# Performance work log

Measured on AMD Instinct MI355X. Metric: run time of the kernel, lower is better.

Reference implementation:

```python
import jax, jax.numpy as jnp
import numpy as np

B, C, N = 4, 128, 25000
E = 200000            # edges per graph
H, DH = 4, 32         # heads, per-head dim
OUT = H * DH          # 128
ED = 32               # edge feature dim


def setup_inputs() -> dict:
    key = jax.random.key(0)
    ks = jax.random.split(key, 16)
    s = 0.05
    return {
        'x': jax.random.normal(ks[0], (B, C, N, 1), jnp.float32),
        'edge_index': jax.random.randint(ks[1], (B, 2, E), 0, B * N, jnp.int64),
        'edge_attr': jax.random.normal(ks[2], (B * E, ED), jnp.float32),
        'Wq': jax.random.normal(ks[3], (C, OUT), jnp.float32) * s,
        'bq': jnp.zeros((OUT,), jnp.float32),
        'Wk': jax.random.normal(ks[4], (C, OUT), jnp.float32) * s,
        'bk': jnp.zeros((OUT,), jnp.float32),
        'Wv': jax.random.normal(ks[5], (C, OUT), jnp.float32) * s,
        'bv': jnp.zeros((OUT,), jnp.float32),
        'We': jax.random.normal(ks[6], (ED, OUT), jnp.float32) * s,
        'Wskip': jax.random.normal(ks[7], (C, OUT), jnp.float32) * s,
        'bskip': jnp.zeros((OUT,), jnp.float32),
        'W1': jax.random.normal(ks[8], (OUT, 2 * OUT), jnp.float32) * s,
        'b1': jnp.zeros((2 * OUT,), jnp.float32),
        'W2': jax.random.normal(ks[9], (2 * OUT, OUT), jnp.float32) * s,
        'b2': jnp.zeros((OUT,), jnp.float32),
    }


def reference(x, edge_index, edge_attr, Wq, bq, Wk, bk, Wv, bv, We,
              Wskip, bskip, W1, b1, W2, b2):
    b, c, n, _ = x.shape
    nb = b * n
    # [B,C,N,1] -> [B*N, C]
    xf = x.squeeze(-1).transpose(0, 2, 1).reshape(nb, c)
    # [B,2,E] -> [2, B*E]
    ei = edge_index.transpose(1, 0, 2).reshape(2, -1)
    src, dst = ei[0], ei[1]

    q = (xf @ Wq + bq).reshape(nb, H, DH)
    k = (xf @ Wk + bk).reshape(nb, H, DH)
    v = (xf @ Wv + bv).reshape(nb, H, DH)
    e = (edge_attr @ We).reshape(-1, H, DH)  # [T,H,DH]

    qi = q[dst]            # gather target queries  [T,H,DH]
    kj = k[src] + e        # gather source keys + edge proj
    vj = v[src] + e

    scale = 1.0 / np.sqrt(DH).astype(np.float32)
    alpha = (qi * kj).sum(-1) * scale  # [T,H]

    # segment softmax over edges sharing a destination node
    amax = jax.ops.segment_max(alpha, dst, num_segments=nb)
    amax = jnp.where(jnp.isfinite(amax), amax, 0.0)
    ea = jnp.exp(alpha - amax[dst])
    denom = jax.ops.segment_sum(ea, dst, num_segments=nb)
    attn = ea / (denom[dst] + 1e-16)   # [T,H]

    agg = jax.ops.segment_sum(vj * attn[..., None], dst, num_segments=nb)
    out = agg.reshape(nb, OUT) + (xf @ Wskip + bskip)  # root skip

    # feed-forward + final activation
    h = jnp.maximum(out @ W1 + b1, 0.0) @ W2 + b2
    h = jnp.maximum(h, 0.0)

    # [B*N, OUT] -> [B, OUT, N, 1]
    return h.reshape(b, n, OUT).transpose(0, 2, 1)[..., None]
```

## Files before the change

kernel.cpp:

```cpp
#include <hip/hip_runtime.h>
#include <hip/hip_bf16.h>

#define NB      100000
#define NPB     25000
#define T_E     800000
#define EPG     200000
#define DMODEL  128
#define EDIM    32
#define FFD     256
#define SCAN_NBLK 98

typedef __attribute__((ext_vector_type(8))) short bf16x8;
typedef __attribute__((ext_vector_type(4))) float f32x4;
typedef __attribute__((ext_vector_type(2))) float f32x2;

__device__ inline unsigned short f2bf(float f) {
    unsigned u = __float_as_uint(f);
    unsigned r = u + 0x7fffu + ((u >> 16) & 1u);
    return (unsigned short)(r >> 16);
}
__device__ inline unsigned pack_bf16x2(float lo, float hi) {
    return (unsigned)f2bf(lo) | ((unsigned)f2bf(hi) << 16);
}
__device__ inline float bf_lo(unsigned p) { return __uint_as_float(p << 16); }
__device__ inline float bf_hi(unsigned p) { return __uint_as_float(p & 0xffff0000u); }

__global__ __launch_bounds__(256) void k_prep(
    const float* __restrict__ W1, const float* __restrict__ W2,
    const float* __restrict__ We,
    const float* __restrict__ Wq, const float* __restrict__ Wk,
    const float* __restrict__ Wv, const float* __restrict__ Wskip,
    uint4* __restrict__ w1f, uint4* __restrict__ w2f,
    uint4* __restrict__ wef, uint4* __restrict__ wpf)
{
    int t = blockIdx.x * 256 + threadIdx.x;
    int lane = t & 63;
    int frag = t >> 6;
    if (frag >= 264) return;
    int rl = lane & 15, g = lane >> 4;
    unsigned v[4];
    if (frag < 64) {
        int m1 = frag >> 2, ks = frag & 3;
        int col1 = m1 * 16 + rl;
        int k0 = ks * 32 + g * 8;
#pragma unroll
        for (int j2 = 0; j2 < 4; ++j2) {
            float f0 = W1[(k0 + 2 * j2) * FFD + col1];
            float f1 = W1[(k0 + 2 * j2 + 1) * FFD + col1];
            v[j2] = pack_bf16x2(f0, f1);
        }
        w1f[frag * 64 + lane] = make_uint4(v[0], v[1], v[2], v[3]);
    } else if (frag < 128) {
        int f2 = frag - 64;
        int m2 = f2 >> 3, ks = f2 & 7;
        int c2 = m2 * 16 + rl;
        int k0 = ks * 32 + g * 8;
#pragma unroll
        for (int j2 = 0; j2 < 4; ++j2) {
            float f0 = W2[(k0 + 2 * j2) * DMODEL + c2];
            float f1 = W2[(k0 + 2 * j2 + 1) * DMODEL + c2];
            v[j2] = pack_bf16x2(f0, f1);
        }
        w2f[f2 * 64 + lane] = make_uint4(v[0], v[1], v[2], v[3]);
    } else if (frag < 136) {
        int m = frag - 128;
        int ocol = m * 16 + rl;
        int k0 = g * 8;
#pragma unroll
        for (int j2 = 0; j2 < 4; ++j2) {
            float f0 = We[(k0 + 2 * j2) * DMODEL + ocol];
            float f1 = We[(k0 + 2 * j2 + 1) * DMODEL + ocol];
            v[j2] = pack_bf16x2(f0, f1);
        }
        wef[m * 64 + lane] = make_uint4(v[0], v[1], v[2], v[3]);
    } else {
        int fi = frag - 136;
        int m  = fi >> 5;
        int r  = fi & 31;
        int ct = r >> 2, ks = r & 3;
        const float* W = (m == 0) ? Wq : (m == 1) ? Wk : (m == 2) ? Wv : Wskip;
        int col = ct * 16 + rl;
        int k0  = ks * 32 + g * 8;
#pragma unroll
        for (int j2 = 0; j2 < 4; ++j2) {
            float f0 = W[(k0 + 2 * j2) * DMODEL + col];
            float f1 = W[(k0 + 2 * j2 + 1) * DMODEL + col];
            v[j2] = pack_bf16x2(f0, f1);
        }
        wpf[fi * 64 + lane] = make_uint4(v[0], v[1], v[2], v[3]);
    }
}

__global__ __launch_bounds__(256) void k_proj2(
    const float* __restrict__ x, const uint4* __restrict__ wpf,
    const float* __restrict__ bq, const float* __restrict__ bk,
    const float* __restrict__ bv, const float* __restrict__ bskip,
    unsigned short* __restrict__ qb16, unsigned short* __restrict__ kvb,
    unsigned short* __restrict__ skipb16)
{
    __shared__ __align__(16) char lds[16384];
    const int tid   = threadIdx.x;
    const int node0 = blockIdx.x * 64;

    {
        const int nl   = tid & 63;
        const int half = tid >> 6;
        const int node = node0 + nl;
        const bool valid = node < NB;
        int b  = node / NPB;
        int nn = node - b * NPB;
        const float* xbase = x + (size_t)b * DMODEL * NPB + nn;
#pragma unroll
        for (int o = 0; o < 4; ++o) {
            int c0 = (half * 4 + o) * 8;
            unsigned vals[4];
#pragma unroll
            for (int j2 = 0; j2 < 4; ++j2) {
                float f0 = valid ? xbase[(size_t)(c0 + 2 * j2) * NPB] : 0.f;
                float f1 = valid ? xbase[(size_t)(c0 + 2 * j2 + 1) * NPB] : 0.f;
                vals[j2] = pack_bf16x2(f0, f1);
            }
            int byte = nl * 256 + ((c0 * 2) ^ ((nl & 7) << 4));
            *(uint4*)(&lds[byte]) = make_uint4(vals[0], vals[1], vals[2], vals[3]);
        }
    }
    __syncthreads();

    const int w = tid >> 6, lane = tid & 63;
    const int rl = lane & 15, g = lane >> 4;

    const uint4* wf = wpf + (size_t)w * 32 * 64;
    const float* bi = (w == 0) ? bq : (w == 1) ? bk : (w == 2) ? bv : bskip;
    unsigned short* base = (w == 0) ? qb16 : (w == 3) ? skipb16
                          : kvb + ((w == 2) ? 128 : 0);
    const int rowstride = (w == 1 || w == 2) ? 256 : 128;

#pragma unroll
    for (int ct = 0; ct < 8; ++ct) {
        bf16x8 A[4];
#pragma unroll
        for (int ks = 0; ks < 4; ++ks)
            A[ks] = *(const bf16x8*)&wf[(ct * 4 + ks) * 64 + lane];
        const int colb = ct * 16 + g * 4;
        const float bb0 = bi[colb], bb1 = bi[colb + 1],
                    bb2 = bi[colb + 2], bb3 = bi[colb + 3];
#pragma unroll
        for (int nt = 0; nt < 4; ++nt) {
            const int nl = nt * 16 + rl;
            f32x4 acc = {0.f, 0.f, 0.f, 0.f};
#pragma unroll
            for (int ks = 0; ks < 4; ++ks) {
                bf16x8 B = *(const bf16x8*)(&lds[nl * 256 +
                              ((ks * 64 + g * 16) ^ ((nl & 7) << 4))]);
                acc = __builtin_amdgcn_mfma_f32_16x16x32_bf16(A[ks], B, acc, 0, 0, 0);
            }
            const int node = node0 + nl;
            if (node < NB) {
                unsigned lo = pack_bf16x2(acc[0] + bb0, acc[1] + bb1);
                unsigned hi = pack_bf16x2(acc[2] + bb2, acc[3] + bb3);
                *(uint2*)&base[(size_t)node * rowstride + colb] = make_uint2(lo, hi);
            }
        }
    }
}

__global__ __launch_bounds__(256) void k_hist(
    const int* __restrict__ eidx, int* __restrict__ counts)
{
    int t = blockIdx.x * 256 + threadIdx.x;
    if (t < T_E) {
        int b = t / EPG, e = t - b * EPG;
        int dst = eidx[(size_t)(b * 2 + 1) * EPG + e];
        atomicAdd(&counts[dst], 1);
    }
}

__global__ __launch_bounds__(1024) void k_scan1(
    const int* __restrict__ counts, int* __restrict__ row_start,
    int* __restrict__ bsum)
{
    __shared__ int s[1024];
    const int tid = threadIdx.x;
    const int gid = blockIdx.x * 1024 + tid;
    int v = (gid < NB) ? counts[gid] : 0;
    s[tid] = v;
    __syncthreads();
#pragma unroll
    for (int off = 1; off < 1024; off <<= 1) {
        int tv = (tid >= off) ? s[tid - off] : 0;
        __syncthreads();
        s[tid] += tv;
        __syncthreads();
    }
    int incl = s[tid];
    if (gid < NB) row_start[gid] = incl - v;
    if (tid == 1023) bsum[blockIdx.x] = incl;
}

__global__ __launch_bounds__(128) void k_scan2(int* __restrict__ bsum)
{
    __shared__ int s[128];
    const int tid = threadIdx.x;
    int v = (tid < SCAN_NBLK) ? bsum[tid] : 0;
    s[tid] = v;
    __syncthreads();
#pragma unroll
    for (int off = 1; off < 128; off <<= 1) {
        int tv = (tid >= off) ? s[tid - off] : 0;
        __syncthreads();
        s[tid] += tv;
        __syncthreads();
    }
    if (tid < SCAN_NBLK) bsum[tid] = s[tid] - v;
}

__global__ __launch_bounds__(1024) void k_scan3(
    int* __restrict__ row_start, const int* __restrict__ bsum,
    int* __restrict__ cursor)
{
    const int gid = blockIdx.x * 1024 + threadIdx.x;
    if (gid < NB) {
        int v = row_start[gid] + bsum[blockIdx.x];
        row_start[gid] = v;
        cursor[gid] = v;
    }
}

__global__ __launch_bounds__(256) void k_scatter(
    const int* __restrict__ eidx, int* __restrict__ cursor,
    int2* __restrict__ elist2)
{
    int t = blockIdx.x * 256 + threadIdx.x;
    if (t < T_E) {
        int b = t / EPG, e = t - b * EPG;
        int dst = eidx[(size_t)(b * 2 + 1) * EPG + e];
        int src = eidx[(size_t)(b * 2) * EPG + e];
        int pos = atomicAdd(&cursor[dst], 1);
        elist2[pos] = make_int2(src, t);
    }
}

__global__ __launch_bounds__(256) void k_eproj(
    const float* __restrict__ eattr, const uint4* __restrict__ wef,
    unsigned char* __restrict__ eb)
{
    const int tid = threadIdx.x;
    const int w = tid >> 6, lane = tid & 63;
    const int rl = lane & 15, g = lane >> 4;

    bf16x8 a[8];
#pragma unroll
    for (int m = 0; m < 8; ++m) a[m] = *(const bf16x8*)&wef[m * 64 + lane];

    const int nwaves = gridDim.x * 4;
    for (int tile = blockIdx.x * 4 + w; tile < T_E / 16; tile += nwaves) {
        const float* ep = &eattr[((size_t)tile * 16 + rl) * EDIM + g * 8];
        float4 f0 = *(const float4*)ep;
        float4 f1 = *(const float4*)(ep + 4);
        uint4 bu = make_uint4(pack_bf16x2(f0.x, f0.y), pack_bf16x2(f0.z, f0.w),
                              pack_bf16x2(f1.x, f1.y), pack_bf16x2(f1.z, f1.w));
        bf16x8 b = *(bf16x8*)&bu;
        f32x4 z = {0.f, 0.f, 0.f, 0.f};
        f32x4 acc[8];
#pragma unroll
        for (int m = 0; m < 8; ++m)
            acc[m] = __builtin_amdgcn_mfma_f32_16x16x32_bf16(a[m], b, z, 0, 0, 0);
        unsigned char* out = &eb[((size_t)tile * 16 + rl) * DMODEL + g * 4];
#pragma unroll
        for (int m = 0; m < 8; ++m) {
            unsigned d = __builtin_amdgcn_cvt_pk_fp8_f32(acc[m][0], acc[m][1], 0, false);
            d = __builtin_amdgcn_cvt_pk_fp8_f32(acc[m][2], acc[m][3], d, true);
            *(unsigned*)(out + m * 16) = d;
        }
    }
}

__global__ __launch_bounds__(256) void k_aggr3(
    unsigned short* qx,
    const unsigned short* __restrict__ kvb,
    const unsigned short* __restrict__ skipb16,
    const unsigned char* __restrict__ eb,
    const int2* __restrict__ elist2,
    const int* __restrict__ row_start, const int* __restrict__ row_end)
{
    const int tid = threadIdx.x;
    const int w = tid >> 6, l = tid & 63;
    const int q4 = l >> 4;
    const int li = l & 15;
    const int c0 = li * 8;

    const int nwaves = gridDim.x * 4;
    for (int node = blockIdx.x * 4 + w; node < NB; node += nwaves) {
        const int rs = row_start[node];
        const int re = row_end[node];
        uint4 qp = *(const uint4*)&qx[(size_t)node * DMODEL + c0];
        const float q0 = bf_lo(qp.x), q1 = bf_hi(qp.x);
        const float q2 = bf_lo(qp.y), q3 = bf_hi(qp.y);
        const float q4_ = bf_lo(qp.z), q5 = bf_hi(qp.z);
        const float q6 = bf_lo(qp.w), q7 = bf_hi(qp.w);
        float a0 = 0.f, a1 = 0.f, a2 = 0.f, a3 = 0.f;
        float a4 = 0.f, a5 = 0.f, a6 = 0.f, a7 = 0.f, den = 0.f;

        for (int j0 = rs; j0 < re; j0 += 4) {
            const int jc = j0 + q4;
            const bool act = jc < re;
            uint4 kp = make_uint4(0, 0, 0, 0), vp = make_uint4(0, 0, 0, 0);
            uint2 ep8 = make_uint2(0, 0);
            if (act) {
                int2 se = elist2[jc];
                kp = *(const uint4*)&kvb[(size_t)se.x * 256 + c0];
                vp = *(const uint4*)&kvb[(size_t)se.x * 256 + 128 + c0];
                ep8 = *(const uint2*)&eb[(size_t)se.y * DMODEL + c0];
            }
            f32x2 exl = __builtin_amdgcn_cvt_pk_f32_fp8(ep8.x, false);
            f32x2 exh = __builtin_amdgcn_cvt_pk_f32_fp8(ep8.x, true);
            f32x2 eyl = __builtin_amdgcn_cvt_pk_f32_fp8(ep8.y, false);
            f32x2 eyh = __builtin_amdgcn_cvt_pk_f32_fp8(ep8.y, true);
            const float e0 = exl[0], e1 = exl[1], e2 = exh[0], e3 = exh[1];
            const float e4 = eyl[0], e5 = eyl[1], e6 = eyh[0], e7 = eyh[1];
            const float k0 = bf_lo(kp.x) + e0, k1 = bf_hi(kp.x) + e1;
            const float k2 = bf_lo(kp.y) + e2, k3 = bf_hi(kp.y) + e3;
            const float k4 = bf_lo(kp.z) + e4, k5 = bf_hi(kp.z) + e5;
            const float k6 = bf_lo(kp.w) + e6, k7 = bf_hi(kp.w) + e7;
            float p = q0 * k0 + q1 * k1 + q2 * k2 + q3 * k3
                    + q4_ * k4 + q5 * k5 + q6 * k6 + q7 * k7;
            p += __shfl_xor(p, 1, 64);
            p += __shfl_xor(p, 2, 64);
            float ea = act ? __expf(p * 0.17677669529663689f) : 0.f;
            a0 += ea * (bf_lo(vp.x) + e0);
            a1 += ea * (bf_hi(vp.x) + e1);
            a2 += ea * (bf_lo(vp.y) + e2);
            a3 += ea * (bf_hi(vp.y) + e3);
            a4 += ea * (bf_lo(vp.z) + e4);
            a5 += ea * (bf_hi(vp.z) + e5);
            a6 += ea * (bf_lo(vp.w) + e6);
            a7 += ea * (bf_hi(vp.w) + e7);
            den += ea;
        }
#pragma unroll
        for (int off = 16; off <= 32; off <<= 1) {
            a0 += __shfl_xor(a0, off, 64);
            a1 += __shfl_xor(a1, off, 64);
            a2 += __shfl_xor(a2, off, 64);
            a3 += __shfl_xor(a3, off, 64);
            a4 += __shfl_xor(a4, off, 64);
            a5 += __shfl_xor(a5, off, 64);
            a6 += __shfl_xor(a6, off, 64);
            a7 += __shfl_xor(a7, off, 64);
            den += __shfl_xor(den, off, 64);
        }
        float r = 1.0f / (den + 1e-16f);
        if (q4 == 0) {
            uint4 sp = *(const uint4*)&skipb16[(size_t)node * DMODEL + c0];
            uint4 o;
            o.x = pack_bf16x2(a0 * r + bf_lo(sp.x), a1 * r + bf_hi(sp.x));
            o.y = pack_bf16x2(a2 * r + bf_lo(sp.y), a3 * r + bf_hi(sp.y));
            o.z = pack_bf16x2(a4 * r + bf_lo(sp.z), a5 * r + bf_hi(sp.z));
            o.w = pack_bf16x2(a6 * r + bf_lo(sp.w), a7 * r + bf_hi(sp.w));
            *(uint4*)&qx[(size_t)node * DMODEL + c0] = o;
        }
    }
}

#define H1_OFF 16384

__global__ __launch_bounds__(256) void k_ffn_mfma(
    const unsigned short* __restrict__ xs16,
    const uint4* __restrict__ w1f, const float* __restrict__ b1,
    const uint4* __restrict__ w2f, const float* __restrict__ b2,
    float* __restrict__ out)
{
    __shared__ __align__(16) char lds[49152];
    const int tid   = threadIdx.x;
    const int node0 = blockIdx.x * 64;

#pragma unroll
    for (int i = 0; i < 4; ++i) {
        int linear = i * 256 + tid;
        int row = linear >> 4;
        int c8  = (linear & 15) * 8;
        int node = node0 + row;
        uint4 vv = (node < NB) ? *(const uint4*)&xs16[(size_t)node * DMODEL + c8]
                               : make_uint4(0, 0, 0, 0);
        int byte = row * 256 + ((c8 * 2) ^ ((row & 7) << 4));
        *(uint4*)(&lds[byte]) = vv;
    }
    __syncthreads();

    const int w = tid >> 6, lane = tid & 63;
    const int rl = lane & 15, g = lane >> 4;

    {
        f32x4 acc[4][4] = {};
#pragma unroll
        for (int ks = 0; ks < 4; ++ks) {
            bf16x8 a[4], b[4];
#pragma unroll
            for (int mt = 0; mt < 4; ++mt) {
                int m1 = w * 4 + mt;
                a[mt] = *(const bf16x8*)&w1f[(m1 * 4 + ks) * 64 + lane];
            }
#pragma unroll
            for (int nt = 0; nt < 4; ++nt) {
                int node = nt * 16 + rl;
                int byte = node * 256 + ((ks * 64 + g * 16) ^ ((node & 7) << 4));
                b[nt] = *(const bf16x8*)&lds[byte];
            }
#pragma unroll
            for (int mt = 0; mt < 4; ++mt)
#pragma unroll
                for (int nt = 0; nt < 4; ++nt)
                    acc[mt][nt] = __builtin_amdgcn_mfma_f32_16x16x32_bf16(
                        a[mt], b[nt], acc[mt][nt], 0, 0, 0);
        }
#pragma unroll
        for (int mt = 0; mt < 4; ++mt) {
            int col1_0 = w * 64 + mt * 16 + g * 4;
            float bb0 = b1[col1_0], bb1 = b1[col1_0 + 1],
                  bb2 = b1[col1_0 + 2], bb3 = b1[col1_0 + 3];
#pragma unroll
            for (int nt = 0; nt < 4; ++nt) {
                int node = nt * 16 + rl;
                float v0 = fmaxf(acc[mt][nt][0] + bb0, 0.f);
                float v1 = fmaxf(acc[mt][nt][1] + bb1, 0.f);
                float v2 = fmaxf(acc[mt][nt][2] + bb2, 0.f);
                float v3 = fmaxf(acc[mt][nt][3] + bb3, 0.f);
                unsigned lo = pack_bf16x2(v0, v1), hi = pack_bf16x2(v2, v3);
                int byte = H1_OFF + node * 512 + ((col1_0 * 2) ^ ((node & 7) << 4));
                *(uint2*)(&lds[byte]) = make_uint2(lo, hi);
            }
        }
    }
    __syncthreads();

    {
        f32x4 acc[2][4] = {};
#pragma unroll
        for (int ks = 0; ks < 8; ++ks) {
            bf16x8 a[2], b[4];
#pragma unroll
            for (int mt = 0; mt < 2; ++mt) {
                int m2 = w * 2 + mt;
                a[mt] = *(const bf16x8*)&w2f[(m2 * 8 + ks) * 64 + lane];
            }
#pragma unroll
            for (int nt = 0; nt < 4; ++nt) {
                int node = nt * 16 + rl;
                int byte = H1_OFF + node * 512 + ((ks * 64 + g * 16) ^ ((node & 7) << 4));
                b[nt] = *(const bf16x8*)&lds[byte];
            }
#pragma unroll
            for (int mt = 0; mt < 2; ++mt)
#pragma unroll
                for (int nt = 0; nt < 4; ++nt)
                    acc[mt][nt] = __builtin_amdgcn_mfma_f32_16x16x32_bf16(
                        a[mt], b[nt], acc[mt][nt], 0, 0, 0);
        }
#pragma unroll
        for (int mt = 0; mt < 2; ++mt) {
            int c2_0 = w * 32 + mt * 16 + g * 4;
#pragma unroll
            for (int nt = 0; nt < 4; ++nt) {
                int node = node0 + nt * 16 + rl;
                if (node < NB) {
                    int bb = node / NPB;
                    int nn = node - bb * NPB;
                    size_t base = (size_t)(bb * DMODEL) * NPB + nn;
#pragma unroll
                    for (int r = 0; r < 4; ++r) {
                        float v = fmaxf(acc[mt][nt][r] + b2[c2_0 + r], 0.f);
                        out[base + (size_t)(c2_0 + r) * NPB] = v;
                    }
                }
            }
        }
    }
}

extern "C" void kernel_launch(void* const* d_in, const int* in_sizes, int n_in,
                              void* d_out, int out_size, void* d_ws, size_t ws_size,
                              hipStream_t stream)
{
    const float* x     = (const float*)d_in[0];
    const int*   eidx  = (const int*)  d_in[1];
    const float* eattr = (const float*)d_in[2];
    const float* Wq    = (const float*)d_in[3];
    const float* bq    = (const float*)d_in[4];
    const float* Wk    = (const float*)d_in[5];
    const float* bk    = (const float*)d_in[6];
    const float* Wv    = (const float*)d_in[7];
    const float* bv    = (const float*)d_in[8];
    const float* We    = (const float*)d_in[9];
    const float* Wskip = (const float*)d_in[10];
    const float* bskip = (const float*)d_in[11];
    const float* W1    = (const float*)d_in[12];
    const float* b1    = (const float*)d_in[13];
    const float* W2    = (const float*)d_in[14];
    const float* b2    = (const float*)d_in[15];
    float* out = (float*)d_out;

    const size_t NBD = (size_t)NB * DMODEL;
    unsigned short* qb16    = (unsigned short*)d_ws;
    unsigned short* kvb     = qb16 + NBD;
    unsigned short* skipb16 = kvb + 2 * NBD;
    unsigned char*  eb      = (unsigned char*)(skipb16 + NBD);
    uint4* w1f = (uint4*)(eb + (size_t)T_E * DMODEL);
    uint4* w2f = w1f + 64 * 64;
    uint4* wef = w2f + 64 * 64;
    uint4* wpf = wef + 8 * 64;
    int* counts    = (int*)(wpf + 128 * 64);
    int* row_start = counts + NB;
    int* cursor    = row_start + NB;
    int2* elist2   = (int2*)(cursor + NB);
    int* bsum      = (int*)(elist2 + T_E);

    hipMemsetAsync(counts, 0, NB * sizeof(int), stream);
    k_prep<<<66, 256, 0, stream>>>(W1, W2, We, Wq, Wk, Wv, Wskip,
                                   w1f, w2f, wef, wpf);
    k_proj2<<<(NB + 63) / 64, 256, 0, stream>>>(x, wpf, bq, bk, bv, bskip,
                                                qb16, kvb, skipb16);
    k_hist<<<(T_E + 255) / 256, 256, 0, stream>>>(eidx, counts);
    k_scan1<<<SCAN_NBLK, 1024, 0, stream>>>(counts, row_start, bsum);
    k_scan2<<<1, 128, 0, stream>>>(bsum);
    k_scan3<<<SCAN_NBLK, 1024, 0, stream>>>(row_start, bsum, cursor);
    k_scatter<<<(T_E + 255) / 256, 256, 0, stream>>>(eidx, cursor, elist2);
    k_eproj<<<2048, 256, 0, stream>>>(eattr, wef, eb);
    k_aggr3<<<2048, 256, 0, stream>>>(qb16, kvb, skipb16, eb, elist2,
                                      row_start, cursor);
    k_ffn_mfma<<<(NB + 63) / 64, 256, 0, stream>>>(qb16, w1f, b1, w2f, b2, out);
}
```

Measured before the change: 369.1 us.

## Stage projection outputs in LDS, fuse edge scatter into eproj, unroll aggregation

```diff
diff --git a/kernel.cpp b/kernel.cpp
--- a/kernel.cpp
+++ b/kernel.cpp
@@ -91,6 +91,8 @@
     }
 }
 
+#define STG 16384
+
 __global__ __launch_bounds__(256) void k_proj2(
     const float* __restrict__ x, const uint4* __restrict__ wpf,
     const float* __restrict__ bq, const float* __restrict__ bk,
@@ -98,7 +100,7 @@
     unsigned short* __restrict__ qb16, unsigned short* __restrict__ kvb,
     unsigned short* __restrict__ skipb16)
 {
-    __shared__ __align__(16) char lds[16384];
+    __shared__ __align__(16) char lds[32768];
     const int tid   = threadIdx.x;
     const int node0 = blockIdx.x * 64;
 
@@ -129,38 +131,51 @@
     const int w = tid >> 6, lane = tid & 63;
     const int rl = lane & 15, g = lane >> 4;
 
-    const uint4* wf = wpf + (size_t)w * 32 * 64;
-    const float* bi = (w == 0) ? bq : (w == 1) ? bk : (w == 2) ? bv : bskip;
-    unsigned short* base = (w == 0) ? qb16 : (w == 3) ? skipb16
-                          : kvb + ((w == 2) ? 128 : 0);
-    const int rowstride = (w == 1 || w == 2) ? 256 : 128;
-
-#pragma unroll
-    for (int ct = 0; ct < 8; ++ct) {
-        bf16x8 A[4];
-#pragma unroll
-        for (int ks = 0; ks < 4; ++ks)
-            A[ks] = *(const bf16x8*)&wf[(ct * 4 + ks) * 64 + lane];
-        const int colb = ct * 16 + g * 4;
-        const float bb0 = bi[colb], bb1 = bi[colb + 1],
-                    bb2 = bi[colb + 2], bb3 = bi[colb + 3];
-#pragma unroll
-        for (int nt = 0; nt < 4; ++nt) {
-            const int nl = nt * 16 + rl;
-            f32x4 acc = {0.f, 0.f, 0.f, 0.f};
-#pragma unroll
-            for (int ks = 0; ks < 4; ++ks) {
-                bf16x8 B = *(const bf16x8*)(&lds[nl * 256 +
-                              ((ks * 64 + g * 16) ^ ((nl & 7) << 4))]);
-                acc = __builtin_amdgcn_mfma_f32_16x16x32_bf16(A[ks], B, acc, 0, 0, 0);
-            }
-            const int node = node0 + nl;
-            if (node < NB) {
+    for (int m = 0; m < 4; ++m) {
+        const float* bi = (m == 0) ? bq : (m == 1) ? bk : (m == 2) ? bv : bskip;
+#pragma unroll
+        for (int ct2 = 0; ct2 < 2; ++ct2) {
+            const int ct = w * 2 + ct2;
+            bf16x8 A[4];
+#pragma unroll
+            for (int ks = 0; ks < 4; ++ks)
+                A[ks] = *(const bf16x8*)&wpf[((m * 8 + ct) * 4 + ks) * 64 + lane];
+            const int colb = ct * 16 + g * 4;
+            const float bb0 = bi[colb], bb1 = bi[colb + 1],
+                        bb2 = bi[colb + 2], bb3 = bi[colb + 3];
+#pragma unroll
+            for (int nt = 0; nt < 4; ++nt) {
+                const int nl = nt * 16 + rl;
+                f32x4 acc = {0.f, 0.f, 0.f, 0.f};
+#pragma unroll
+                for (int ks = 0; ks < 4; ++ks) {
+                    bf16x8 B = *(const bf16x8*)(&lds[nl * 256 +
+                                  ((ks * 64 + g * 16) ^ ((nl & 7) << 4))]);
+                    acc = __builtin_amdgcn_mfma_f32_16x16x32_bf16(A[ks], B, acc, 0, 0, 0);
+                }
                 unsigned lo = pack_bf16x2(acc[0] + bb0, acc[1] + bb1);
                 unsigned hi = pack_bf16x2(acc[2] + bb2, acc[3] + bb3);
-                *(uint2*)&base[(size_t)node * rowstride + colb] = make_uint2(lo, hi);
-            }
-        }
+                int byte = STG + nl * 256 + ((colb * 2) ^ ((nl & 7) << 4));
+                *(uint2*)(&lds[byte]) = make_uint2(lo, hi);
+            }
+        }
+        __syncthreads();
+#pragma unroll
+        for (int i = 0; i < 4; ++i) {
+            int linear = i * 256 + tid;
+            int row = linear >> 4;
+            int c8  = (linear & 15) * 8;
+            int node = node0 + row;
+            if (node < NB) {
+                uint4 vv = *(const uint4*)(&lds[STG + row * 256 +
+                                ((c8 * 2) ^ ((row & 7) << 4))]);
+                if (m == 0)      *(uint4*)&qb16[(size_t)node * DMODEL + c8] = vv;
+                else if (m == 1) *(uint4*)&kvb[(size_t)node * 256 + c8] = vv;
+                else if (m == 2) *(uint4*)&kvb[(size_t)node * 256 + 128 + c8] = vv;
+                else             *(uint4*)&skipb16[(size_t)node * DMODEL + c8] = vv;
+            }
+        }
+        __syncthreads();
     }
 }
 
@@ -226,23 +241,10 @@
     }
 }
 
-__global__ __launch_bounds__(256) void k_scatter(
+__global__ __launch_bounds__(256) void k_escat(
+    const float* __restrict__ eattr, const uint4* __restrict__ wef,
     const int* __restrict__ eidx, int* __restrict__ cursor,
-    int2* __restrict__ elist2)
-{
-    int t = blockIdx.x * 256 + threadIdx.x;
-    if (t < T_E) {
-        int b = t / EPG, e = t - b * EPG;
-        int dst = eidx[(size_t)(b * 2 + 1) * EPG + e];
-        int src = eidx[(size_t)(b * 2) * EPG + e];
-        int pos = atomicAdd(&cursor[dst], 1);
-        elist2[pos] = make_int2(src, t);
-    }
-}
-
-__global__ __launch_bounds__(256) void k_eproj(
-    const float* __restrict__ eattr, const uint4* __restrict__ wef,
-    unsigned char* __restrict__ eb)
+    unsigned char* __restrict__ eb, int2* __restrict__ elist2)
 {
     const int tid = threadIdx.x;
     const int w = tid >> 6, lane = tid & 63;
@@ -271,6 +273,14 @@
             unsigned d = __builtin_amdgcn_cvt_pk_fp8_f32(acc[m][0], acc[m][1], 0, false);
             d = __builtin_amdgcn_cvt_pk_fp8_f32(acc[m][2], acc[m][3], d, true);
             *(unsigned*)(out + m * 16) = d;
+        }
+        if (g == 0) {
+            int t = tile * 16 + rl;
+            int bb = t / EPG, e = t - bb * EPG;
+            int dst = eidx[(size_t)(bb * 2 + 1) * EPG + e];
+            int src = eidx[(size_t)(bb * 2) * EPG + e];
+            int pos = atomicAdd(&cursor[dst], 1);
+            elist2[pos] = make_int2(src, t);
         }
     }
 }
@@ -301,52 +311,73 @@
         float a0 = 0.f, a1 = 0.f, a2 = 0.f, a3 = 0.f;
         float a4 = 0.f, a5 = 0.f, a6 = 0.f, a7 = 0.f, den = 0.f;
 
-        for (int j0 = rs; j0 < re; j0 += 4) {
-            const int jc = j0 + q4;
-            const bool act = jc < re;
-            uint4 kp = make_uint4(0, 0, 0, 0), vp = make_uint4(0, 0, 0, 0);
-            uint2 ep8 = make_uint2(0, 0);
-            if (act) {
-                int2 se = elist2[jc];
-                kp = *(const uint4*)&kvb[(size_t)se.x * 256 + c0];
-                vp = *(const uint4*)&kvb[(size_t)se.x * 256 + 128 + c0];
-                ep8 = *(const uint2*)&eb[(size_t)se.y * DMODEL + c0];
-            }
-            f32x2 exl = __builtin_amdgcn_cvt_pk_f32_fp8(ep8.x, false);
-            f32x2 exh = __builtin_amdgcn_cvt_pk_f32_fp8(ep8.x, true);
-            f32x2 eyl = __builtin_amdgcn_cvt_pk_f32_fp8(ep8.y, false);
-            f32x2 eyh = __builtin_amdgcn_cvt_pk_f32_fp8(ep8.y, true);
-            const float e0 = exl[0], e1 = exl[1], e2 = exh[0], e3 = exh[1];
-            const float e4 = eyl[0], e5 = eyl[1], e6 = eyh[0], e7 = eyh[1];
-            const float k0 = bf_lo(kp.x) + e0, k1 = bf_hi(kp.x) + e1;
-            const float k2 = bf_lo(kp.y) + e2, k3 = bf_hi(kp.y) + e3;
-            const float k4 = bf_lo(kp.z) + e4, k5 = bf_hi(kp.z) + e5;
-            const float k6 = bf_lo(kp.w) + e6, k7 = bf_hi(kp.w) + e7;
-            float p = q0 * k0 + q1 * k1 + q2 * k2 + q3 * k3
-                    + q4_ * k4 + q5 * k5 + q6 * k6 + q7 * k7;
-            p += __shfl_xor(p, 1, 64);
-            p += __shfl_xor(p, 2, 64);
-            float ea = act ? __expf(p * 0.17677669529663689f) : 0.f;
-            a0 += ea * (bf_lo(vp.x) + e0);
-            a1 += ea * (bf_hi(vp.x) + e1);
-            a2 += ea * (bf_lo(vp.y) + e2);
-            a3 += ea * (bf_hi(vp.y) + e3);
-            a4 += ea * (bf_lo(vp.z) + e4);
-            a5 += ea * (bf_hi(vp.z) + e5);
-            a6 += ea * (bf_lo(vp.w) + e6);
-            a7 += ea * (bf_hi(vp.w) + e7);
-            den += ea;
+        for (int j0 = rs; j0 < re; j0 += 8) {
+            const int jcA = j0 + q4;
+            const int jcB = j0 + 4 + q4;
+            const bool actA = jcA < re;
+            const bool actB = jcB < re;
+            uint4 kpA = make_uint4(0,0,0,0), vpA = make_uint4(0,0,0,0);
+            uint4 kpB = make_uint4(0,0,0,0), vpB = make_uint4(0,0,0,0);
+            uint2 epA = make_uint2(0,0), epB = make_uint2(0,0);
+            if (actA) {
+                int2 se = elist2[jcA];
+                kpA = *(const uint4*)&kvb[(size_t)se.x * 256 + c0];
+                vpA = *(const uint4*)&kvb[(size_t)se.x * 256 + 128 + c0];
+                epA = *(const uint2*)&eb[(size_t)se.y * DMODEL + c0];
+            }
+            if (actB) {
+                int2 se = elist2[jcB];
+                kpB = *(const uint4*)&kvb[(size_t)se.x * 256 + c0];
+                vpB = *(const uint4*)&kvb[(size_t)se.x * 256 + 128 + c0];
+                epB = *(const uint2*)&eb[(size_t)se.y * DMODEL + c0];
+            }
+            {
+                f32x2 exl = __builtin_amdgcn_cvt_pk_f32_fp8(epA.x, false);
+                f32x2 exh = __builtin_amdgcn_cvt_pk_f32_fp8(epA.x, true);
+                f32x2 eyl = __builtin_amdgcn_cvt_pk_f32_fp8(epA.y, false);
+                f32x2 eyh = __builtin_amdgcn_cvt_pk_f32_fp8(epA.y, true);
+                const float e0 = exl[0], e1 = exl[1], e2 = exh[0], e3 = exh[1];
+                const float e4 = eyl[0], e5 = eyl[1], e6 = eyh[0], e7 = eyh[1];
+                float p = q0 * (bf_lo(kpA.x) + e0) + q1 * (bf_hi(kpA.x) + e1)
+                        + q2 * (bf_lo(kpA.y) + e2) + q3 * (bf_hi(kpA.y) + e3)
+                        + q4_ * (bf_lo(kpA.z) + e4) + q5 * (bf_hi(kpA.z) + e5)
+                        + q6 * (bf_lo(kpA.w) + e6) + q7 * (bf_hi(kpA.w) + e7);
+                p += __shfl_xor(p, 1, 64);
+                p += __shfl_xor(p, 2, 64);
+                float ea = actA ? __expf(p * 0.17677669529663689f) : 0.f;
+                a0 += ea * (bf_lo(vpA.x) + e0);  a1 += ea * (bf_hi(vpA.x) + e1);
+                a2 += ea * (bf_lo(vpA.y) + e2);  a3 += ea * (bf_hi(vpA.y) + e3);
+                a4 += ea * (bf_lo(vpA.z) + e4);  a5 += ea * (bf_hi(vpA.z) + e5);
+                a6 += ea * (bf_lo(vpA.w) + e6);  a7 += ea * (bf_hi(vpA.w) + e7);
+                den += ea;
+            }
+            {
+                f32x2 exl = __builtin_amdgcn_cvt_pk_f32_fp8(epB.x, false);
+                f32x2 exh = __builtin_amdgcn_cvt_pk_f32_fp8(epB.x, true);
+                f32x2 eyl = __builtin_amdgcn_cvt_pk_f32_fp8(epB.y, false);
+                f32x2 eyh = __builtin_amdgcn_cvt_pk_f32_fp8(epB.y, true);
+                const float e0 = exl[0], e1 = exl[1], e2 = exh[0], e3 = exh[1];
+                const float e4 = eyl[0], e5 = eyl[1], e6 = eyh[0], e7 = eyh[1];
+                float p = q0 * (bf_lo(kpB.x) + e0) + q1 * (bf_hi(kpB.x) + e1)
+                        + q2 * (bf_lo(kpB.y) + e2) + q3 * (bf_hi(kpB.y) + e3)
+                        + q4_ * (bf_lo(kpB.z) + e4) + q5 * (bf_hi(kpB.z) + e5)
+                        + q6 * (bf_lo(kpB.w) + e6) + q7 * (bf_hi(kpB.w) + e7);
+                p += __shfl_xor(p, 1, 64);
+                p += __shfl_xor(p, 2, 64);
+                float ea = actB ? __expf(p * 0.17677669529663689f) : 0.f;
+                a0 += ea * (bf_lo(vpB.x) + e0);  a1 += ea * (bf_hi(vpB.x) + e1);
+                a2 += ea * (bf_lo(vpB.y) + e2);  a3 += ea * (bf_hi(vpB.y) + e3);
+                a4 += ea * (bf_lo(vpB.z) + e4);  a5 += ea * (bf_hi(vpB.z) + e5);
+                a6 += ea * (bf_lo(vpB.w) + e6);  a7 += ea * (bf_hi(vpB.w) + e7);
+                den += ea;
+            }
         }
 #pragma unroll
         for (int off = 16; off <= 32; off <<= 1) {
-            a0 += __shfl_xor(a0, off, 64);
-            a1 += __shfl_xor(a1, off, 64);
-            a2 += __shfl_xor(a2, off, 64);
-            a3 += __shfl_xor(a3, off, 64);
-            a4 += __shfl_xor(a4, off, 64);
-            a5 += __shfl_xor(a5, off, 64);
-            a6 += __shfl_xor(a6, off, 64);
-            a7 += __shfl_xor(a7, off, 64);
+            a0 += __shfl_xor(a0, off, 64);  a1 += __shfl_xor(a1, off, 64);
+            a2 += __shfl_xor(a2, off, 64);  a3 += __shfl_xor(a3, off, 64);
+            a4 += __shfl_xor(a4, off, 64);  a5 += __shfl_xor(a5, off, 64);
+            a6 += __shfl_xor(a6, off, 64);  a7 += __shfl_xor(a7, off, 64);
             den += __shfl_xor(den, off, 64);
         }
         float r = 1.0f / (den + 1e-16f);
@@ -523,8 +554,7 @@
     k_scan1<<<SCAN_NBLK, 1024, 0, stream>>>(counts, row_start, bsum);
     k_scan2<<<1, 128, 0, stream>>>(bsum);
     k_scan3<<<SCAN_NBLK, 1024, 0, stream>>>(row_start, bsum, cursor);
-    k_scatter<<<(T_E + 255) / 256, 256, 0, stream>>>(eidx, cursor, elist2);
-    k_eproj<<<2048, 256, 0, stream>>>(eattr, wef, eb);
+    k_escat<<<2048, 256, 0, stream>>>(eattr, wef, eidx, cursor, eb, elist2);
     k_aggr3<<<2048, 256, 0, stream>>>(qb16, kvb, skipb16, eb, elist2,
                                       row_start, cursor);
     k_ffn_mfma<<<(NB + 63) / 64, 256, 0, stream>>>(qb16, w1f, b1, w2f, b2, out);
```

New measurement: 340.3 us. 7.8% less time.
